# Kernel tuning notes

Hardware: AMD Instinct MI355X
Metric: run time of the kernel (lower is better)

The kernel has to match this reference:

```python
import jax, jax.numpy as jnp
import numpy as np

N = 262144          # active voxels
C_IN = 64
C_OUT = 64
BATCH = 2
D0, D1, D2 = 128, 128, 128   # sparse spatial grid
VOL = D0 * D1 * D2


def setup_inputs() -> dict:
    key = jax.random.key(0)
    kf, kw = jax.random.split(key, 2)
    # unique voxel coordinates (submanifold conv assumes no duplicate sites)
    rng = np.random.default_rng(0)
    packed = rng.choice(BATCH * VOL, size=N, replace=False)
    b = packed // VOL
    r = packed % VOL
    i0 = r // (D1 * D2)
    r2 = r % (D1 * D2)
    i1 = r2 // D2
    i2 = r2 % D2
    indices = jnp.asarray(np.stack([b, i0, i1, i2], axis=1), dtype=jnp.int32)  # [N,4]
    features = jax.random.normal(kf, (N, C_IN), dtype=jnp.float32)
    # KRSC layout: [out_ch, k0, k1, k2, in_ch], trunc_normal(std=0.02) ~ normal here
    weight = jax.random.normal(kw, (C_OUT, 3, 3, 3, C_IN), dtype=jnp.float32) * 0.02
    bias = jnp.zeros((C_OUT,), dtype=jnp.float32)
    return {"features": features, "weight": weight, "bias": bias, "indices": indices}


def reference(features, weight, bias, indices):
    n = features.shape[0]
    idx = indices.astype(jnp.int32)
    # linearize (b, i0, i1, i2); packing is linear in coords so neighbor pack = pack + shift
    packed = idx[:, 0] * VOL + idx[:, 1] * (D1 * D2) + idx[:, 2] * D2 + idx[:, 3]
    order = jnp.argsort(packed)
    sorted_pack = packed[order]
    out = jnp.zeros((n, C_OUT), dtype=features.dtype)
    for k0 in range(3):
        for k1 in range(3):
            for k2 in range(3):
                shift = (k0 - 1) * (D1 * D2) + (k1 - 1) * D2 + (k2 - 1)
                neigh_pack = packed + shift
                p = jnp.searchsorted(sorted_pack, neigh_pack)
                pc = jnp.minimum(p, n - 1)
                ok = (p < n) & (sorted_pack[pc] == neigh_pack)
                src = jnp.where(ok, order[pc], 0)
                gathered = jnp.where(ok[:, None], features[src], 0.0)  # [N, C_in]
                out = out + gathered @ weight[:, k0, k1, k2, :].T      # [N, C_out]
    return out + bias
```

## Files before the change

### kernel.cpp

```cpp
#include <hip/hip_runtime.h>

#define VOL   2097152
#define TBL   4194304
#define D1D2  16384
#define DD2   128
#define TILE  128

typedef __bf16 bf16_t;
typedef bf16_t bf16x8 __attribute__((ext_vector_type(8)));
typedef float  floatx4 __attribute__((ext_vector_type(4)));


__global__ __launch_bounds__(256) void prep_k(const float* __restrict__ w,
                                              const int* __restrict__ idx,
                                              int* __restrict__ table,
                                              bf16_t* __restrict__ wb, int n) {
    const int b = blockIdx.x;
    const int tblB = (n + 255) >> 8;
    if (b < tblB) {
        int t = b * 256 + threadIdx.x;
        if (t < n) {
            int4 c = ((const int4*)idx)[t];
            int p = ((c.x * 128 + c.y) * 128 + c.z) * 128 + c.w;
            table[p] = t;
        }
    } else {
        int t = (b - tblB) * 256 + threadIdx.x;
        if (t < 27 * 64 * 64) {
            int ci = t & 63, co = (t >> 6) & 63, k = t >> 12;
            wb[t] = (bf16_t)w[(co * 27 + k) * 64 + ci];
        }
    }
}


__global__ __launch_bounds__(256) void count_k(const int* __restrict__ table,
                                               int* __restrict__ rc) {
    __shared__ int s[256];
    const int t = threadIdx.x;
    const int base = blockIdx.x * 4096 + t * 16;
    int c = 0;
    #pragma unroll
    for (int i = 0; i < 4; ++i) {
        int4 v = ((const int4*)(table + base))[i];
        c += (v.x >= 0) + (v.y >= 0) + (v.z >= 0) + (v.w >= 0);
    }
    s[t] = c;
    __syncthreads();
    for (int off = 128; off; off >>= 1) {
        if (t < off) s[t] += s[t + off];
        __syncthreads();
    }
    if (t == 0) rc[blockIdx.x] = s[0];
}

__global__ __launch_bounds__(1024) void scan_k(const int* __restrict__ rc,
                                               int* __restrict__ rb) {
    __shared__ int s[1024];
    const int t = threadIdx.x;
    int v = rc[t];
    s[t] = v;
    __syncthreads();
    int x = v;
    for (int off = 1; off < 1024; off <<= 1) {
        int y = (t >= off) ? s[t - off] : 0;
        __syncthreads();
        x += y;
        s[t] = x;
        __syncthreads();
    }
    rb[t] = x - v;
}

__global__ __launch_bounds__(256) void compact_k(int* __restrict__ table,
                                                 int* __restrict__ ord,
                                                 int* __restrict__ pkd,
                                                 const int* __restrict__ rb) {
    __shared__ int s_cnt[256];
    const int t = threadIdx.x;
    const int base = blockIdx.x * 4096 + t * 16;

    int v[16];
    #pragma unroll
    for (int i = 0; i < 4; ++i)
        *(int4*)&v[i * 4] = ((const int4*)(table + base))[i];
    int cnt = 0;
    #pragma unroll
    for (int i = 0; i < 16; ++i) cnt += (v[i] >= 0);

    s_cnt[t] = cnt;
    __syncthreads();
    int x = cnt;
    for (int off = 1; off < 256; off <<= 1) {
        int y = (t >= off) ? s_cnt[t - off] : 0;
        __syncthreads();
        x += y;
        s_cnt[t] = x;
        __syncthreads();
    }

    int pos = rb[blockIdx.x] + x - cnt;
    #pragma unroll
    for (int i = 0; i < 16; ++i) {
        if (v[i] >= 0) {
            ord[pos] = v[i];
            pkd[pos] = base + i;
            table[base + i] = pos;
            ++pos;
        }
    }
}

__global__ void feat_k(const float* __restrict__ f, const int* __restrict__ ord,
                       bf16_t* __restrict__ fbp, int n) {
    int t = blockIdx.x * blockDim.x + threadIdx.x;
    int pos = t >> 3, c = (t & 7) * 8;
    if (pos < n) {
        int orig = ord[pos];
        const float* src = f + (size_t)orig * 64 + c;
        float4 a  = *(const float4*)src;
        float4 b2 = *(const float4*)(src + 4);
        bf16x8 o = { (bf16_t)a.x,  (bf16_t)a.y,  (bf16_t)a.z,  (bf16_t)a.w,
                     (bf16_t)b2.x, (bf16_t)b2.y, (bf16_t)b2.z, (bf16_t)b2.w };
        *(bf16x8*)(fbp + (size_t)pos * 64 + c) = o;
    }
}


__global__ __launch_bounds__(256) void conv_k(
        const bf16_t* __restrict__ fbp, const bf16_t* __restrict__ wb,
        const int* __restrict__ table, const int* __restrict__ pkd,
        const int* __restrict__ ord, const float* __restrict__ bias,
        float* __restrict__ out, int n)
{
    __shared__ int    s_pkd[TILE];
    __shared__ int    s_ord[TILE];
    __shared__ int    s_nbr[27 * TILE];
    __shared__ bf16_t sF[TILE * 72];
    __shared__ bf16_t sW[64 * 72];

    const int t    = threadIdx.x;
    const int tile = blockIdx.x * TILE;

    if (t < TILE) {
        int vn = tile + t;
        s_pkd[t] = (vn < n) ? pkd[vn] : (int)0xC0000000;
        s_ord[t] = (vn < n) ? ord[vn] : 0;
    }
    __syncthreads();

    for (int u = t; u < 27 * TILE; u += 256) {
        int k  = u >> 7;
        int r  = u & (TILE - 1);
        int k0 = k / 9, k1 = (k / 3) % 3, k2 = k % 3;
        int np = s_pkd[r] + (k0 - 1) * D1D2 + (k1 - 1) * DD2 + (k2 - 1);
        s_nbr[u] = (np >= 0 && np < TBL) ? table[np] : -1;
    }

    const int lane = t & 63;
    const int w    = t >> 6;
    const int l15  = lane & 15;
    const int q    = lane >> 4;

    const int rF = t >> 1;
    const int hF = t & 1;
    const int rW = t >> 2;
    const int cW = t & 3;

    floatx4 acc[8] = {};

    __syncthreads();

    bf16x8 pf[4] = {{}, {}, {}, {}};
    bf16x8 pw0, pw1;
    {
        int nbr = s_nbr[rF];
        if (nbr >= 0) {
            const bf16x8* src = (const bf16x8*)(fbp + (size_t)nbr * 64 + hF * 32);
            pf[0] = src[0];
            pf[1] = src[1];
            pf[2] = src[2];
            pf[3] = src[3];
        }
        const bf16x8* wsrc = (const bf16x8*)(wb + rW * 64 + cW * 16);
        pw0 = wsrc[0];
        pw1 = wsrc[1];
    }

    for (int k = 0; k < 27; ++k) {
        *(bf16x8*)&sF[rF * 72 + hF * 32]      = pf[0];
        *(bf16x8*)&sF[rF * 72 + hF * 32 + 8]  = pf[1];
        *(bf16x8*)&sF[rF * 72 + hF * 32 + 16] = pf[2];
        *(bf16x8*)&sF[rF * 72 + hF * 32 + 24] = pf[3];
        *(bf16x8*)&sW[rW * 72 + cW * 16]      = pw0;
        *(bf16x8*)&sW[rW * 72 + cW * 16 + 8]  = pw1;

        if (k + 1 < 27) {
            int nbr = s_nbr[(k + 1) * TILE + rF];
            bf16x8 n0 = {}, n1 = {}, n2 = {}, n3 = {};
            if (nbr >= 0) {
                const bf16x8* src = (const bf16x8*)(fbp + (size_t)nbr * 64 + hF * 32);
                n0 = src[0];
                n1 = src[1];
                n2 = src[2];
                n3 = src[3];
            }
            const bf16x8* wsrc = (const bf16x8*)(wb + ((k + 1) * 64 + rW) * 64 + cW * 16);
            pw0   = wsrc[0];
            pw1   = wsrc[1];
            pf[0] = n0;
            pf[1] = n1;
            pf[2] = n2;
            pf[3] = n3;
        }

        __syncthreads();

        #pragma unroll
        for (int s = 0; s < 2; ++s) {
            bf16x8 a = *(const bf16x8*)&sW[(w * 16 + l15) * 72 + s * 32 + q * 8];
            #pragma unroll
            for (int g = 0; g < 8; ++g) {
                bf16x8 bfrag = *(const bf16x8*)&sF[(g * 16 + l15) * 72 + s * 32 + q * 8];
                acc[g] = __builtin_amdgcn_mfma_f32_16x16x32_bf16(a, bfrag, acc[g], 0, 0, 0);
            }
        }

        __syncthreads();
    }

    float4 bs = *(const float4*)&bias[w * 16 + q * 4];
    #pragma unroll
    for (int g = 0; g < 8; ++g) {
        int vn = tile + g * 16 + l15;
        if (vn < n) {
            int orig = s_ord[g * 16 + l15];
            float4 o;
            o.x = acc[g][0] + bs.x;
            o.y = acc[g][1] + bs.y;
            o.z = acc[g][2] + bs.z;
            o.w = acc[g][3] + bs.w;
            *(float4*)&out[(size_t)orig * 64 + w * 16 + q * 4] = o;
        }
    }
}


extern "C" void kernel_launch(void* const* d_in, const int* in_sizes, int n_in,
                              void* d_out, int out_size, void* d_ws, size_t ws_size,
                              hipStream_t stream) {
    const float* feat = (const float*)d_in[0];
    const float* wgt  = (const float*)d_in[1];
    const float* bias = (const float*)d_in[2];
    const int*   idx  = (const int*)d_in[3];
    float* out = (float*)d_out;

    const int n = in_sizes[0] / 64;

    char* ws = (char*)d_ws;
    int*    table = (int*)ws;
    bf16_t* wbf   = (bf16_t*)(ws + (size_t)TBL * 4);
    bf16_t* fbp   = (bf16_t*)(ws + (size_t)TBL * 4 + 262144);
    int*    ord   = (int*)(ws + (size_t)TBL * 4 + 262144 + (size_t)n * 128);
    int*    pkd   = ord + n;
    int*    rc    = pkd + n;
    int*    rb    = rc + 1024;

    hipMemsetAsync(table, 0xFF, (size_t)TBL * 4, stream);

    int tblB = (n + 255) >> 8;
    prep_k<<<tblB + 432, 256, 0, stream>>>(wgt, idx, table, wbf, n);
    count_k<<<1024, 256, 0, stream>>>(table, rc);
    scan_k<<<1, 1024, 0, stream>>>(rc, rb);
    compact_k<<<1024, 256, 0, stream>>>(table, ord, pkd, rb);

    int nu = n * 8;
    feat_k<<<(nu + 255) / 256, 256, 0, stream>>>(feat, ord, fbp, n);

    conv_k<<<(n + TILE - 1) / TILE, 256, 0, stream>>>(fbp, wbf, table, pkd, ord, bias, out, n);
}
```

Before: 244.9 us.

## Fuse preprocessing kernels and switch conv to 32x32 MFMA with register weights

Counts per-block occupancy with atomics in prep_k (rc memset to -1, compensated by +1), folds count/scan/feature conversion into compact_k via a per-block prefix reduction over rc, cutting four launches to two. The conv kernel drops the shared weight tile and loads weight fragments directly into registers in a pre-swizzled layout, uses 32x32x16 bf16 MFMA with two accumulators per wave, and remaps block indices for locality. This removes launch overhead and LDS weight traffic at the cost of atomics and redundant prefix sums per block.

Result: slower. 276.8 us (+13.0%).

```diff
diff --git a/kernel.cpp b/kernel.cpp
--- a/kernel.cpp
+++ b/kernel.cpp
@@ -8,12 +8,13 @@
 
 typedef __bf16 bf16_t;
 typedef bf16_t bf16x8 __attribute__((ext_vector_type(8)));
-typedef float  floatx4 __attribute__((ext_vector_type(4)));
+typedef float  floatx16 __attribute__((ext_vector_type(16)));
 
 
 __global__ __launch_bounds__(256) void prep_k(const float* __restrict__ w,
                                               const int* __restrict__ idx,
                                               int* __restrict__ table,
+                                              int* __restrict__ rc,
                                               bf16_t* __restrict__ wb, int n) {
     const int b = blockIdx.x;
     const int tblB = (n + 255) >> 8;
@@ -23,63 +24,41 @@
             int4 c = ((const int4*)idx)[t];
             int p = ((c.x * 128 + c.y) * 128 + c.z) * 128 + c.w;
             table[p] = t;
+            atomicAdd(&rc[p >> 12], 1);
         }
     } else {
         int t = (b - tblB) * 256 + threadIdx.x;
         if (t < 27 * 64 * 64) {
-            int ci = t & 63, co = (t >> 6) & 63, k = t >> 12;
-            wb[t] = (bf16_t)w[(co * 27 + k) * 64 + ci];
-        }
-    }
-}
-
-
-__global__ __launch_bounds__(256) void count_k(const int* __restrict__ table,
-                                               int* __restrict__ rc) {
-    __shared__ int s[256];
-    const int t = threadIdx.x;
-    const int base = blockIdx.x * 4096 + t * 16;
-    int c = 0;
-    #pragma unroll
-    for (int i = 0; i < 4; ++i) {
-        int4 v = ((const int4*)(table + base))[i];
-        c += (v.x >= 0) + (v.y >= 0) + (v.z >= 0) + (v.w >= 0);
-    }
-    s[t] = c;
-    __syncthreads();
-    for (int off = 128; off; off >>= 1) {
-        if (t < off) s[t] += s[t + off];
-        __syncthreads();
-    }
-    if (t == 0) rc[blockIdx.x] = s[0];
-}
-
-__global__ __launch_bounds__(1024) void scan_k(const int* __restrict__ rc,
-                                               int* __restrict__ rb) {
-    __shared__ int s[1024];
-    const int t = threadIdx.x;
-    int v = rc[t];
-    s[t] = v;
-    __syncthreads();
-    int x = v;
-    for (int off = 1; off < 1024; off <<= 1) {
-        int y = (t >= off) ? s[t - off] : 0;
-        __syncthreads();
-        x += y;
-        s[t] = x;
-        __syncthreads();
-    }
-    rb[t] = x - v;
-}
-
-__global__ __launch_bounds__(256) void compact_k(int* __restrict__ table,
+            int j = t & 7, co = (t >> 3) & 63, cb = (t >> 9) & 7, tap = t >> 12;
+            wb[t] = (bf16_t)w[(co * 27 + tap) * 64 + cb * 8 + j];
+        }
+    }
+}
+
+
+__global__ __launch_bounds__(256) void compact_k(const float* __restrict__ f,
+                                                 int* __restrict__ table,
+                                                 const int* __restrict__ rc,
                                                  int* __restrict__ ord,
                                                  int* __restrict__ pkd,
-                                                 const int* __restrict__ rb) {
+                                                 bf16_t* __restrict__ fbp) {
+    __shared__ int s_red[256];
     __shared__ int s_cnt[256];
-    const int t = threadIdx.x;
-    const int base = blockIdx.x * 4096 + t * 16;
-
+    __shared__ int s_orig[4096];
+    const int t   = threadIdx.x;
+    const int bid = blockIdx.x;
+
+    int part = 0;
+    for (int i = t; i < bid; i += 256) part += rc[i] + 1;
+    s_red[t] = part;
+    __syncthreads();
+    for (int off = 128; off; off >>= 1) {
+        if (t < off) s_red[t] += s_red[t + off];
+        __syncthreads();
+    }
+    const int rbase = s_red[0];
+
+    const int base = bid * 4096 + t * 16;
     int v[16];
     #pragma unroll
     for (int i = 0; i < 4; ++i)
@@ -99,30 +78,30 @@
         __syncthreads();
     }
 
-    int pos = rb[blockIdx.x] + x - cnt;
+    int lp = x - cnt;
+    int pos = rbase + lp;
     #pragma unroll
     for (int i = 0; i < 16; ++i) {
         if (v[i] >= 0) {
             ord[pos] = v[i];
             pkd[pos] = base + i;
             table[base + i] = pos;
-            ++pos;
-        }
-    }
-}
-
-__global__ void feat_k(const float* __restrict__ f, const int* __restrict__ ord,
-                       bf16_t* __restrict__ fbp, int n) {
-    int t = blockIdx.x * blockDim.x + threadIdx.x;
-    int pos = t >> 3, c = (t & 7) * 8;
-    if (pos < n) {
-        int orig = ord[pos];
+            s_orig[lp] = v[i];
+            ++lp; ++pos;
+        }
+    }
+    __syncthreads();
+
+    const int total = s_cnt[255];
+    for (int u = t; u < total * 8; u += 256) {
+        int vox = u >> 3, c = (u & 7) * 8;
+        int orig = s_orig[vox];
         const float* src = f + (size_t)orig * 64 + c;
         float4 a  = *(const float4*)src;
         float4 b2 = *(const float4*)(src + 4);
         bf16x8 o = { (bf16_t)a.x,  (bf16_t)a.y,  (bf16_t)a.z,  (bf16_t)a.w,
                      (bf16_t)b2.x, (bf16_t)b2.y, (bf16_t)b2.z, (bf16_t)b2.w };
-        *(bf16x8*)(fbp + (size_t)pos * 64 + c) = o;
+        *(bf16x8*)(fbp + (size_t)(rbase + vox) * 64 + c) = o;
     }
 }
 
@@ -137,10 +116,12 @@
     __shared__ int    s_ord[TILE];
     __shared__ int    s_nbr[27 * TILE];
     __shared__ bf16_t sF[TILE * 72];
-    __shared__ bf16_t sW[64 * 72];
-
-    const int t    = threadIdx.x;
-    const int tile = blockIdx.x * TILE;
+
+    const int t  = threadIdx.x;
+    int bidx = blockIdx.x;
+    int gb = gridDim.x;
+    if ((gb & 7) == 0) bidx = (bidx & 7) * (gb >> 3) + (bidx >> 3);
+    const int tile = bidx * TILE;
 
     if (t < TILE) {
         int vn = tile + t;
@@ -159,32 +140,29 @@
 
     const int lane = t & 63;
     const int w    = t >> 6;
-    const int l15  = lane & 15;
-    const int q    = lane >> 4;
+    const int ct   = w & 1;
+    const int vh   = (w >> 1) * 64;
+    const int l31  = lane & 31;
+    const int h    = lane >> 5;
 
     const int rF = t >> 1;
     const int hF = t & 1;
-    const int rW = t >> 2;
-    const int cW = t & 3;
-
-    floatx4 acc[8] = {};
+
+    floatx16 acc0 = {}, acc1 = {};
 
     __syncthreads();
 
     bf16x8 pf[4] = {{}, {}, {}, {}};
-    bf16x8 pw0, pw1;
+    bf16x8 pa[4];
     {
         int nbr = s_nbr[rF];
         if (nbr >= 0) {
             const bf16x8* src = (const bf16x8*)(fbp + (size_t)nbr * 64 + hF * 32);
-            pf[0] = src[0];
-            pf[1] = src[1];
-            pf[2] = src[2];
-            pf[3] = src[3];
-        }
-        const bf16x8* wsrc = (const bf16x8*)(wb + rW * 64 + cW * 16);
-        pw0 = wsrc[0];
-        pw1 = wsrc[1];
+            pf[0] = src[0]; pf[1] = src[1]; pf[2] = src[2]; pf[3] = src[3];
+        }
+        #pragma unroll
+        for (int ks = 0; ks < 4; ++ks)
+            pa[ks] = *(const bf16x8*)(wb + ((ks * 2 + h) * 64 + ct * 32 + l31) * 8);
     }
 
     for (int k = 0; k < 27; ++k) {
@@ -192,55 +170,63 @@
         *(bf16x8*)&sF[rF * 72 + hF * 32 + 8]  = pf[1];
         *(bf16x8*)&sF[rF * 72 + hF * 32 + 16] = pf[2];
         *(bf16x8*)&sF[rF * 72 + hF * 32 + 24] = pf[3];
-        *(bf16x8*)&sW[rW * 72 + cW * 16]      = pw0;
-        *(bf16x8*)&sW[rW * 72 + cW * 16 + 8]  = pw1;
-
-        if (k + 1 < 27) {
+
+        bf16x8 nf[4] = {{}, {}, {}, {}};
+        bf16x8 na[4];
+        const bool more = (k + 1 < 27);
+        if (more) {
             int nbr = s_nbr[(k + 1) * TILE + rF];
-            bf16x8 n0 = {}, n1 = {}, n2 = {}, n3 = {};
             if (nbr >= 0) {
                 const bf16x8* src = (const bf16x8*)(fbp + (size_t)nbr * 64 + hF * 32);
-                n0 = src[0];
-                n1 = src[1];
-                n2 = src[2];
-                n3 = src[3];
+                nf[0] = src[0]; nf[1] = src[1]; nf[2] = src[2]; nf[3] = src[3];
             }
-            const bf16x8* wsrc = (const bf16x8*)(wb + ((k + 1) * 64 + rW) * 64 + cW * 16);
-            pw0   = wsrc[0];
-            pw1   = wsrc[1];
-            pf[0] = n0;
-            pf[1] = n1;
-            pf[2] = n2;
-            pf[3] = n3;
+            #pragma unroll
+            for (int ks = 0; ks < 4; ++ks)
+                na[ks] = *(const bf16x8*)(wb +
+                          (((k + 1) * 8 + ks * 2 + h) * 64 + ct * 32 + l31) * 8);
         }
 
         __syncthreads();
 
         #pragma unroll
-        for (int s = 0; s < 2; ++s) {
-            bf16x8 a = *(const bf16x8*)&sW[(w * 16 + l15) * 72 + s * 32 + q * 8];
+        for (int ks = 0; ks < 4; ++ks) {
+            bf16x8 a  = pa[ks];
+            bf16x8 b0 = *(const bf16x8*)&sF[(vh + l31) * 72      + ks * 16 + h * 8];
+            bf16x8 b1 = *(const bf16x8*)&sF[(vh + 32 + l31) * 72 + ks * 16 + h * 8];
+            acc0 = __builtin_amdgcn_mfma_f32_32x32x16_bf16(a, b0, acc0, 0, 0, 0);
+            acc1 = __builtin_amdgcn_mfma_f32_32x32x16_bf16(a, b1, acc1, 0, 0, 0);
+        }
+
+        __syncthreads();
+
+        if (more) {
             #pragma unroll
-            for (int g = 0; g < 8; ++g) {
-                bf16x8 bfrag = *(const bf16x8*)&sF[(g * 16 + l15) * 72 + s * 32 + q * 8];
-                acc[g] = __builtin_amdgcn_mfma_f32_16x16x32_bf16(a, bfrag, acc[g], 0, 0, 0);
+            for (int i = 0; i < 4; ++i) { pf[i] = nf[i]; pa[i] = na[i]; }
+        }
+    }
+
+    float4 b4[4];
+    #pragma unroll
+    for (int rg = 0; rg < 4; ++rg)
+        b4[rg] = *(const float4*)&bias[ct * 32 + h * 4 + rg * 8];
+
+    #pragma unroll
+    for (int vt = 0; vt < 2; ++vt) {
+        int vl = vh + vt * 32 + l31;
+        int vn = tile + vl;
+        if (vn < n) {
+            int orig = s_ord[vl];
+            float* dst = out + (size_t)orig * 64 + ct * 32 + h * 4;
+            floatx16 A = vt ? acc1 : acc0;
+            #pragma unroll
+            for (int rg = 0; rg < 4; ++rg) {
+                float4 o;
+                o.x = A[rg * 4 + 0] + b4[rg].x;
+                o.y = A[rg * 4 + 1] + b4[rg].y;
+                o.z = A[rg * 4 + 2] + b4[rg].z;
+                o.w = A[rg * 4 + 3] + b4[rg].w;
+                *(float4*)(dst + rg * 8) = o;
             }
-        }
-
-        __syncthreads();
-    }
-
-    float4 bs = *(const float4*)&bias[w * 16 + q * 4];
-    #pragma unroll
-    for (int g = 0; g < 8; ++g) {
-        int vn = tile + g * 16 + l15;
-        if (vn < n) {
-            int orig = s_ord[g * 16 + l15];
-            float4 o;
-            o.x = acc[g][0] + bs.x;
-            o.y = acc[g][1] + bs.y;
-            o.z = acc[g][2] + bs.z;
-            o.w = acc[g][3] + bs.w;
-            *(float4*)&out[(size_t)orig * 64 + w * 16 + q * 4] = o;
         }
     }
 }
@@ -259,23 +245,16 @@
 
     char* ws = (char*)d_ws;
     int*    table = (int*)ws;
-    bf16_t* wbf   = (bf16_t*)(ws + (size_t)TBL * 4);
-    bf16_t* fbp   = (bf16_t*)(ws + (size_t)TBL * 4 + 262144);
-    int*    ord   = (int*)(ws + (size_t)TBL * 4 + 262144 + (size_t)n * 128);
+    int*    rc    = (int*)(ws + (size_t)TBL * 4);
+    bf16_t* wbf   = (bf16_t*)(ws + (size_t)TBL * 4 + 4096);
+    bf16_t* fbp   = (bf16_t*)(ws + (size_t)TBL * 4 + 4096 + 262144);
+    int*    ord   = (int*)(ws + (size_t)TBL * 4 + 4096 + 262144 + (size_t)n * 128);
     int*    pkd   = ord + n;
-    int*    rc    = pkd + n;
-    int*    rb    = rc + 1024;
-
-    hipMemsetAsync(table, 0xFF, (size_t)TBL * 4, stream);
+
+    hipMemsetAsync(table, 0xFF, (size_t)TBL * 4 + 4096, stream);
 
     int tblB = (n + 255) >> 8;
-    prep_k<<<tblB + 432, 256, 0, stream>>>(wgt, idx, table, wbf, n);
-    count_k<<<1024, 256, 0, stream>>>(table, rc);
-    scan_k<<<1, 1024, 0, stream>>>(rc, rb);
-    compact_k<<<1024, 256, 0, stream>>>(table, ord, pkd, rb);
-
-    int nu = n * 8;
-    feat_k<<<(nu + 255) / 256, 256, 0, stream>>>(feat, ord, fbp, n);
-
+    prep_k<<<tblB + 432, 256, 0, stream>>>(wgt, idx, table, rc, wbf, n);
+    compact_k<<<1024, 256, 0, stream>>>(feat, table, rc, ord, pkd, fbp);
     conv_k<<<(n + TILE - 1) / TILE, 256, 0, stream>>>(fbp, wbf, table, pkd, ord, bias, out, n);
 }
```
